# Kernel optimization log

Measured on AMD Instinct MI355X. Metric: run time of the kernel, lower is better.

## Reference

```python
import jax, jax.numpy as jnp
from jax import lax
import numpy as np

HIDDEN = 40
NUM_LAYERS = 7
B, H, W = 16, 64, 64
KS = 7
PAD = KS // 2  # 3

# mask for conv_2d type 'A': zero rows below center, zero right-of-center in
# the center row, and zero the center tap itself
_m = np.ones((1, 1, KS, KS), np.float32)
_m[:, :, PAD + 1:, :] = 0
_m[:, :, PAD, PAD + 1:] = 0
_m[:, :, PAD, PAD] = 0
MASK_A = jnp.asarray(_m)


def conv2d(x, w, pad):
    return lax.conv_general_dilated(x, w, (1, 1), pad,
                                    dimension_numbers=('NCHW', 'OIHW', 'NCHW'))


def setup_inputs() -> dict:
    key = jax.random.key(0)
    ks = jax.random.split(key, 12)
    s = 0.05
    return {
        'input_tensor': jax.random.normal(ks[0], (B, 1, H, W), jnp.float32),
        'target_tensor': jax.random.normal(ks[1], (B, 1, H, W), jnp.float32),
        # masked conv_2d(7,1,80) applied to target
        'w_is': jax.random.normal(ks[2], (2 * HIDDEN, 1, KS, KS), jnp.float32) * s,
        'b_is': jnp.ones((2 * HIDDEN,), jnp.float32),
        # conv_i_s: Conv2d(1, 80, 7, pad 3)
        'w_cis': jax.random.normal(ks[3], (2 * HIDDEN, 1, KS, KS), jnp.float32) * s,
        'b_cis': jax.random.normal(ks[4], (2 * HIDDEN,), jnp.float32) * s,
        # row convs: Conv2d(40, 40, [1,3], pad [0,1])
        'w_rh': jax.random.normal(ks[5], (HIDDEN, HIDDEN, 1, 3), jnp.float32) * s,
        'b_rh': jax.random.normal(ks[6], (HIDDEN,), jnp.float32) * s,
        'w_rc': jax.random.normal(ks[7], (HIDDEN, HIDDEN, 1, 3), jnp.float32) * s,
        'b_rc': jax.random.normal(ks[8], (HIDDEN,), jnp.float32) * s,
        # per-layer cell 1x1 convs: 40 -> 160, stacked over layers
        'w_cell': jax.random.normal(ks[9], (NUM_LAYERS, 4 * HIDDEN, HIDDEN), jnp.float32) * s,
        'b_cell': jax.random.normal(ks[10], (NUM_LAYERS, 4 * HIDDEN), jnp.float32) * s,
        # conv_out: Conv2d(40, 256, 1)
        'w_out': jax.random.normal(ks[11], (256, HIDDEN), jnp.float32) * s,
        'b_out': jnp.zeros((256,), jnp.float32),
    }


def reference(input_tensor, target_tensor, w_is, b_is, w_cis, b_cis,
              w_rh, b_rh, w_rc, b_rc, w_cell, b_cell, w_out, b_out):
    same7 = ((PAD, PAD), (PAD, PAD))
    # i_s = cat([conv_i_s(input), masked_conv(target)], dim=1) -> [B, 160, H, W]
    i_s_input = conv2d(input_tensor, w_cis, same7) + b_cis[None, :, None, None]
    i_s_target = conv2d(target_tensor, w_is * MASK_A, same7) + b_is[None, :, None, None]
    i_s = jnp.concatenate([i_s_input, i_s_target], axis=1)

    h0 = jnp.zeros((B, HIDDEN, 1, W), i_s.dtype)
    c0 = jnp.zeros((B, HIDDEN, 1, W), i_s.dtype)

    def step(carry, x_t):  # x_t: [B, 160, 1, W]
        h, c = carry
        h = conv2d(h, w_rh, ((0, 0), (1, 1))) + b_rh[None, :, None, None]
        c = conv2d(c, w_rc, ((0, 0), (1, 1))) + b_rc[None, :, None, None]
        for l in range(NUM_LAYERS):
            h_conv = jnp.einsum('oc,bcrw->borw', w_cell[l], h) + b_cell[l][None, :, None, None]
            combined = x_t + h_conv
            cc_i, cc_f, cc_o, cc_g = jnp.split(combined, 4, axis=1)
            i = jax.nn.sigmoid(cc_i)
            f = jax.nn.sigmoid(cc_f)
            o = jax.nn.sigmoid(cc_o)
            g = jnp.tanh(cc_g)
            c = f * c + i * g
            h = o * jnp.tanh(c)
        return (h, c), h

    xs = jnp.moveaxis(i_s, 2, 0)[:, :, :, None, :]  # [H, B, 160, 1, W]
    _, hs = lax.scan(step, (h0, c0), xs)            # hs: [H, B, 40, 1, W]
    hidden = jnp.moveaxis(hs[:, :, :, 0, :], 0, 2)  # [B, 40, H, W]
    out = jnp.einsum('oc,bchw->bohw', w_out, hidden) + b_out[None, :, None, None]
    return jax.nn.relu(out)
```

## Files before the change

kernel.cpp:

```cpp
#include <hip/hip_runtime.h>


typedef __bf16 bf16x8 __attribute__((ext_vector_type(8)));
typedef __bf16 bf16x4 __attribute__((ext_vector_type(4)));
typedef float  f32x4  __attribute__((ext_vector_type(4)));

#define SC1 (-1.44269504089f)
#define SC2 (-2.88539008178f)

#define STP 56
#define HLS 896
#define CWS 17

#define BARRIER_LGKM() __asm__ volatile("s_waitcnt lgkmcnt(0)\ns_barrier" ::: "memory")

__global__ __launch_bounds__(256) void prep_kernel(
        const float* __restrict__ wcell, const float* __restrict__ wrh,
        const float* __restrict__ wrc, const float* __restrict__ bcell,
        const float* __restrict__ brh, const float* __restrict__ brc,
        const float* __restrict__ w_out, const float* __restrict__ b_out,
        __bf16* __restrict__ wsA) {
    int i = blockIdx.x * 256 + threadIdx.x;
    if (i >= 137216) return;
    float val = 0.0f;
    if (i < 35840) {
        int j = i & 7, lane = (i >> 3) & 63, lm = i >> 9;
        int mt = lm % 10, l = lm / 10;
        int k = (lane >> 4) * 8 + j, m = lane & 15, r = m & 3;
        int row = r * 40 + 4 * mt + (m >> 2);
        val = wcell[(l * 160 + row) * 40 + k] * (r == 3 ? SC2 : SC1);
    } else if (i < 71680) {
        int i2 = i - 35840;
        int j = i2 & 7, lane = (i2 >> 3) & 63, lm = i2 >> 9;
        int mt = lm % 10, l = lm / 10;
        int k = 32 + (lane >> 4) * 8 + j, m = lane & 15, r = m & 3;
        int row = r * 40 + 4 * mt + (m >> 2);
        float s = (r == 3 ? SC2 : SC1);
        if (k < 40)       val = wcell[(l * 160 + row) * 40 + k] * s;
        else if (k == 40) val = bcell[l * 160 + row] * s;
    } else if (i < 80896) {
        int i3 = i - 71680;
        int j = i3 & 7, lane = (i3 >> 3) & 63, idx = i3 >> 9;
        int mtc = idx % 3, t2 = idx / 3, dx = t2 % 3, cv = t2 / 3;
        int k = (lane >> 4) * 8 + j;
        int ch = 16 * mtc + (lane & 15);
        const float* w = cv ? wrc : wrh;
        if (ch < 40) val = w[(ch * 40 + k) * 3 + dx];
    } else if (i < 90112) {
        int i4 = i - 80896;
        int j = i4 & 7, lane = (i4 >> 3) & 63, idx = i4 >> 9;
        int mtc = idx % 3, t2 = idx / 3, dx = t2 % 3, cv = t2 / 3;
        int k = 32 + (lane >> 4) * 8 + j;
        int ch = 16 * mtc + (lane & 15);
        if (ch < 40) {
            const float* w = cv ? wrc : wrh;
            if (k < 40)                    val = w[(ch * 40 + k) * 3 + dx];
            else if (k == 40 && dx == 1)   val = (cv ? brc : brh)[ch];
        }
    } else if (i < 105472) {
        int i5 = i - 90112;
        int j = i5 & 7, lane = (i5 >> 3) & 63, idx = i5 >> 9;
        int mt = idx % 10, dx = idx / 10;
        int k = (lane >> 4) * 8 + j, m = lane & 15, r = m & 3;
        int row = r * 40 + 4 * mt + (m >> 2);
        float s = (r == 3 ? SC2 : SC1);
        float acc = 0.0f;
        for (int mm = 0; mm < 40; mm++)
            acc = __builtin_fmaf(wcell[row * 40 + mm],
                                 wrh[(mm * 40 + k) * 3 + dx], acc);
        val = acc * s;
    } else if (i < 120832) {
        int i6 = i - 105472;
        int j = i6 & 7, lane = (i6 >> 3) & 63, idx = i6 >> 9;
        int mt = idx % 10, dx = idx / 10;
        int k = 32 + (lane >> 4) * 8 + j, m = lane & 15, r = m & 3;
        int row = r * 40 + 4 * mt + (m >> 2);
        float s = (r == 3 ? SC2 : SC1);
        if (k < 40) {
            float acc = 0.0f;
            for (int mm = 0; mm < 40; mm++)
                acc = __builtin_fmaf(wcell[row * 40 + mm],
                                     wrh[(mm * 40 + k) * 3 + dx], acc);
            val = acc * s;
        } else if (k == 40 && dx == 1) {
            float acc = bcell[row];
            for (int mm = 0; mm < 40; mm++)
                acc = __builtin_fmaf(wcell[row * 40 + mm], brh[mm], acc);
            val = acc * s;
        }
    } else if (i < 129024) {
        int i7 = i - 120832;
        int j = i7 & 7, lane = (i7 >> 3) & 63, ot = i7 >> 9;
        int k = (lane >> 4) * 8 + j;
        int o = ot * 16 + (lane & 15);
        val = w_out[o * 40 + k];
    } else {
        int i8 = i - 129024;
        int j = i8 & 7, lane = (i8 >> 3) & 63, ot = i8 >> 9;
        int k = 32 + (lane >> 4) * 8 + j;
        int o = ot * 16 + (lane & 15);
        if (k < 40)       val = w_out[o * 40 + k];
        else if (k == 40) val = b_out[o];
    }
    wsA[i] = (__bf16)val;
}

__global__ __launch_bounds__(256) void conv7_kernel(
        const float* __restrict__ inp, const float* __restrict__ tgt,
        const float* __restrict__ w_is, const float* __restrict__ b_is,
        const float* __restrict__ w_cis, const float* __restrict__ b_cis,
        float* __restrict__ x_ws) {
    int b = blockIdx.x >> 6, y = blockIdx.x & 63;
    int tid = threadIdx.x, qq = tid >> 6, w = tid & 63;
    const float* ib = inp + b * 4096;
    const float* tb = tgt + b * 4096;
    float pin[7][7], ptg[4][7];
#pragma unroll
    for (int dy = 0; dy < 7; dy++) {
        int yy = y + dy - 3;
#pragma unroll
        for (int dx = 0; dx < 7; dx++) {
            int xx = w + dx - 3;
            bool ok = (yy >= 0 && yy < 64 && xx >= 0 && xx < 64);
            pin[dy][dx] = ok ? ib[yy * 64 + xx] : 0.0f;
            if (dy < 4) ptg[dy][dx] = ok ? tb[yy * 64 + xx] : 0.0f;
        }
    }
    int g = w >> 4, l16 = w & 15;
    for (int j = 0; j < 10; j++) {
        int cc = 4 * j + qq;
        int ccu = __builtin_amdgcn_readfirstlane(cc);
        float a0 = b_cis[ccu], a1 = b_cis[40 + ccu];
        float a2 = b_is[ccu], a3 = b_is[40 + ccu];
        const float* w0 = w_cis + ccu * 49;
        const float* w1 = w_cis + (40 + ccu) * 49;
        const float* w2 = w_is + ccu * 49;
        const float* w3 = w_is + (40 + ccu) * 49;
#pragma unroll
        for (int dy = 0; dy < 7; dy++)
#pragma unroll
            for (int dx = 0; dx < 7; dx++) {
                a0 = __builtin_fmaf(w0[dy * 7 + dx], pin[dy][dx], a0);
                a1 = __builtin_fmaf(w1[dy * 7 + dx], pin[dy][dx], a1);
            }
#pragma unroll
        for (int dy = 0; dy < 3; dy++)
#pragma unroll
            for (int dx = 0; dx < 7; dx++) {
                a2 = __builtin_fmaf(w2[dy * 7 + dx], ptg[dy][dx], a2);
                a3 = __builtin_fmaf(w3[dy * 7 + dx], ptg[dy][dx], a3);
            }
#pragma unroll
        for (int dx = 0; dx < 3; dx++) {
            a2 = __builtin_fmaf(w2[21 + dx], ptg[3][dx], a2);
            a3 = __builtin_fmaf(w3[21 + dx], ptg[3][dx], a3);
        }
        size_t idx = (size_t)((((b * 64 + y) * 4 + g) * 10 + j) * 4 + qq) * 64
                     + l16 * 4;
        *(f32x4*)&x_ws[idx] = f32x4{a0 * SC1, a1 * SC1, a2 * SC1, a3 * SC2};
    }
}

__global__ __launch_bounds__(640, 1) void rnn_kernel(
        const float* __restrict__ x_ws, const __bf16* __restrict__ wsA,
        unsigned long long* __restrict__ halo_ws, float* __restrict__ out) {
    __shared__ __align__(16) __bf16 hC[18 * STP + 64];
    __shared__ __align__(16) __bf16 cC[18 * STP + 64];
    __shared__ __align__(16) __bf16 hL[2 * HLS + 32];
    __shared__ float cwf[40 * CWS];
    __shared__ unsigned cflag[4];

    const int bid = blockIdx.x, g = bid >> 4, b = bid & 15;
    const int tid = threadIdx.x, wv = tid >> 6, lane = tid & 63;
    const int q = lane >> 4, l16 = lane & 15, cc = 4 * wv + q;
    const int W0 = g * 16;

    for (int i = tid; i < 536; i += 640) {
        ((float*)hC)[i] = 0.0f;
        ((float*)cC)[i] = 0.0f;
    }
    for (int i = tid; i < 912; i += 640)
        ((float*)hL)[i] = 0.0f;
    for (int i = tid; i < 40 * CWS; i += 640) cwf[i] = 0.0f;
    if (tid < 4) cflag[tid] = 0xFFFFFFFFu;
    __syncthreads();
    if (tid < 18) { hC[tid * STP + 40] = (__bf16)1.0f; cC[tid * STP + 40] = (__bf16)1.0f; }
    if (tid < 32) hL[(tid >> 4) * HLS + (tid & 15) * STP + 40] = (__bf16)1.0f;
    __syncthreads();

    bf16x8 a0c[6], a1c[6];
#pragma unroll
    for (int l = 1; l < 7; l++) {
        a0c[l - 1] = *(const bf16x8*)&wsA[((l * 10 + wv) * 64 + lane) * 8];
        a1c[l - 1] = *(const bf16x8*)&wsA[35840 + ((l * 10 + wv) * 64 + lane) * 8];
    }
    bf16x8 f0c[3], f1c[3];
#pragma unroll
    for (int dx = 0; dx < 3; dx++) {
        f0c[dx] = *(const bf16x8*)&wsA[90112 + ((dx * 10 + wv) * 64 + lane) * 8];
        f1c[dx] = *(const bf16x8*)&wsA[105472 + ((dx * 10 + wv) * 64 + lane) * 8];
    }
    bf16x8 cva0[3], cva1[3];
    if (wv >= 3 && wv < 6) {
        int mtc = wv - 3;
#pragma unroll
        for (int dx = 0; dx < 3; dx++) {
            int it = (3 + dx) * 3 + mtc;
            cva0[dx] = *(const bf16x8*)&wsA[71680 + (it * 64 + lane) * 8];
            cva1[dx] = *(const bf16x8*)&wsA[80896 + (it * 64 + lane) * 8];
        }
    }
    bf16x8 o0c[2], o1c[2];
    if (wv < 8) {
#pragma unroll
        for (int tt = 0; tt < 2; tt++) {
            int ot = 2 * wv + tt;
            o0c[tt] = *(const bf16x8*)&wsA[120832 + (ot * 64 + lane) * 8];
            o1c[tt] = *(const bf16x8*)&wsA[129024 + (ot * 64 + lane) * 8];
        }
    }

    float c_reg = 0.0f;
    const size_t xstride = 10240;
    const size_t xbase0 = (size_t)(b * 64) * xstride
        + (((size_t)g * 10 + wv) * 4 + q) * 64 + l16 * 4;
    f32x4 xv = *(const f32x4*)&x_ws[xbase0];

    for (int t = 0; t < 64; t++) {
        f32x4 xn = xv;
        if (t < 63) xn = *(const f32x4*)&x_ws[xbase0 + (size_t)(t + 1) * xstride];

        if (wv >= 3 && wv < 6) {
            f32x4 ac = f32x4{0.f, 0.f, 0.f, 0.f};
#pragma unroll
            for (int dx = 0; dx < 3; dx++) {
                bf16x8 b0 = *(const bf16x8*)&cC[(l16 + dx) * STP + q * 8];
                bf16x8 b1 = *(const bf16x8*)&cC[(l16 + dx) * STP + 32 + q * 8];
                ac = __builtin_amdgcn_mfma_f32_16x16x32_bf16(cva0[dx], b0, ac, 0, 0, 0);
                ac = __builtin_amdgcn_mfma_f32_16x16x32_bf16(cva1[dx], b1, ac, 0, 0, 0);
            }
            int mtc = wv - 3, ch0 = 16 * mtc + 4 * q;
            if (ch0 < 40) {
#pragma unroll
                for (int r = 0; r < 4; r++) cwf[(ch0 + r) * CWS + l16] = ac[r];
            }
            __asm__ volatile("s_waitcnt lgkmcnt(0)" ::: "memory");
            if (lane == 0)
                __hip_atomic_store(&cflag[mtc], (unsigned)t,
                                   __ATOMIC_RELAXED, __HIP_MEMORY_SCOPE_WORKGROUP);
        }

        f32x4 acc0 = f32x4{0.f, 0.f, 0.f, 0.f};
#pragma unroll
        for (int dx = 0; dx < 3; dx++) {
            bf16x8 b0 = *(const bf16x8*)&hC[(l16 + dx) * STP + q * 8];
            bf16x8 b1 = *(const bf16x8*)&hC[(l16 + dx) * STP + 32 + q * 8];
            acc0 = __builtin_amdgcn_mfma_f32_16x16x32_bf16(f0c[dx], b0, acc0, 0, 0, 0);
            acc0 = __builtin_amdgcn_mfma_f32_16x16x32_bf16(f1c[dx], b1, acc0, 0, 0, 0);
        }

        if (t > 0 && wv < 8) {
            int y = t - 1;
            bf16x8 bo0 = *(const bf16x8*)&hC[(l16 + 1) * STP + q * 8];
            bf16x8 bo1 = *(const bf16x8*)&hC[(l16 + 1) * STP + 32 + q * 8];
#pragma unroll
            for (int tt = 0; tt < 2; tt++) {
                f32x4 oa = __builtin_amdgcn_mfma_f32_16x16x32_bf16(
                    o0c[tt], bo0, f32x4{0.f, 0.f, 0.f, 0.f}, 0, 0, 0);
                oa = __builtin_amdgcn_mfma_f32_16x16x32_bf16(o1c[tt], bo1, oa, 0, 0, 0);
                int o0 = (2 * wv + tt) * 16 + 4 * q;
#pragma unroll
                for (int r = 0; r < 4; r++)
                    out[((size_t)(b * 256 + o0 + r) * 64 + y) * 64 + W0 + l16] =
                        fmaxf(oa[r], 0.0f);
            }
        }

        {
            int jj = wv >> 2;
            while (__hip_atomic_load(&cflag[jj], __ATOMIC_RELAXED,
                                     __HIP_MEMORY_SCOPE_WORKGROUP) != (unsigned)t)
                __builtin_amdgcn_s_sleep(1);
            __asm__ volatile("" ::: "memory");
        }

#pragma unroll
        for (int l = 0; l < 7; l++) {
            f32x4 acc;
            if (l == 0) {
                acc = acc0;
                c_reg = cwf[cc * CWS + l16];
            } else {
                const __bf16* hb = &hL[(l & 1) * HLS];
                bf16x8 b0 = *(const bf16x8*)&hb[l16 * STP + q * 8];
                bf16x8 b1 = *(const bf16x8*)&hb[l16 * STP + 32 + q * 8];
                acc = __builtin_amdgcn_mfma_f32_16x16x32_bf16(
                    a0c[l - 1], b0, f32x4{0.f, 0.f, 0.f, 0.f}, 0, 0, 0);
                acc = __builtin_amdgcn_mfma_f32_16x16x32_bf16(a1c[l - 1], b1, acc, 0, 0, 0);
            }
            float Ei = __builtin_amdgcn_exp2f(fminf(acc[0] + xv[0], 44.f));
            float Ef = __builtin_amdgcn_exp2f(fminf(acc[1] + xv[1], 44.f));
            float Eo = __builtin_amdgcn_exp2f(fminf(acc[2] + xv[2], 44.f));
            float Eg = __builtin_amdgcn_exp2f(fminf(acc[3] + xv[3], 44.f));
            float f = __builtin_amdgcn_rcpf(1.0f + Ef);
            float ig = (1.0f - Eg) * __builtin_amdgcn_rcpf((1.0f + Ei) * (1.0f + Eg));
            float c = __builtin_fmaf(f, c_reg, ig);
            c_reg = c;
            float Ec = __builtin_amdgcn_exp2f(fminf(SC2 * c, 44.f));
            float h = (1.0f - Ec) * __builtin_amdgcn_rcpf((1.0f + Eo) * (1.0f + Ec));
            if (l < 6) {
                hL[((l + 1) & 1) * HLS + l16 * STP + cc] = (__bf16)h;
                BARRIER_LGKM();
            } else {
                hC[(l16 + 1) * STP + cc] = (__bf16)h;
                cC[(l16 + 1) * STP + cc] = (__bf16)c;
                if (t < 63) {
                    unsigned short h16 = __builtin_bit_cast(unsigned short, (__bf16)h);
                    unsigned short c16 = __builtin_bit_cast(unsigned short, (__bf16)c);
                    unsigned long long v = ((unsigned long long)(unsigned)t << 32)
                        | ((unsigned)c16 << 16) | (unsigned)h16;
                    if (l16 == 0 && g > 0)
                        __hip_atomic_store(
                            &halo_ws[((bid * 2 + 0) * 2 + (t & 1)) * 40 + cc], v,
                            __ATOMIC_RELAXED, __HIP_MEMORY_SCOPE_AGENT);
                    if (l16 == 15 && g < 3)
                        __hip_atomic_store(
                            &halo_ws[((bid * 2 + 1) * 2 + (t & 1)) * 40 + cc], v,
                            __ATOMIC_RELAXED, __HIP_MEMORY_SCOPE_AGENT);
                }
            }
        }

        if (t < 63) {
            if (wv == 8 && g > 0 && lane < 40) {
                const unsigned long long* src =
                    &halo_ws[(((bid - 16) * 2 + 1) * 2 + (t & 1)) * 40 + lane];
                unsigned long long v = __hip_atomic_load(
                    src, __ATOMIC_RELAXED, __HIP_MEMORY_SCOPE_AGENT);
                while ((unsigned)(v >> 32) != (unsigned)t) {
                    __builtin_amdgcn_s_sleep(1);
                    v = __hip_atomic_load(src, __ATOMIC_RELAXED,
                                          __HIP_MEMORY_SCOPE_AGENT);
                }
                hC[lane] = __builtin_bit_cast(__bf16, (unsigned short)(v & 0xffffu));
                cC[lane] = __builtin_bit_cast(__bf16, (unsigned short)((v >> 16) & 0xffffu));
            }
            if (wv == 9 && g < 3 && lane < 40) {
                const unsigned long long* src =
                    &halo_ws[(((bid + 16) * 2 + 0) * 2 + (t & 1)) * 40 + lane];
                unsigned long long v = __hip_atomic_load(
                    src, __ATOMIC_RELAXED, __HIP_MEMORY_SCOPE_AGENT);
                while ((unsigned)(v >> 32) != (unsigned)t) {
                    __builtin_amdgcn_s_sleep(1);
                    v = __hip_atomic_load(src, __ATOMIC_RELAXED,
                                          __HIP_MEMORY_SCOPE_AGENT);
                }
                hC[17 * STP + lane] = __builtin_bit_cast(__bf16, (unsigned short)(v & 0xffffu));
                cC[17 * STP + lane] = __builtin_bit_cast(__bf16, (unsigned short)((v >> 16) & 0xffffu));
            }
        }
        BARRIER_LGKM();
        xv = xn;
    }

    if (wv < 8) {
        bf16x8 bo0 = *(const bf16x8*)&hC[(l16 + 1) * STP + q * 8];
        bf16x8 bo1 = *(const bf16x8*)&hC[(l16 + 1) * STP + 32 + q * 8];
#pragma unroll
        for (int tt = 0; tt < 2; tt++) {
            f32x4 oa = __builtin_amdgcn_mfma_f32_16x16x32_bf16(
                o0c[tt], bo0, f32x4{0.f, 0.f, 0.f, 0.f}, 0, 0, 0);
            oa = __builtin_amdgcn_mfma_f32_16x16x32_bf16(o1c[tt], bo1, oa, 0, 0, 0);
            int o0 = (2 * wv + tt) * 16 + 4 * q;
#pragma unroll
            for (int r = 0; r < 4; r++)
                out[((size_t)(b * 256 + o0 + r) * 64 + 63) * 64 + W0 + l16] =
                    fmaxf(oa[r], 0.0f);
        }
    }
}

extern "C" void kernel_launch(void* const* d_in, const int* in_sizes, int n_in,
                              void* d_out, int out_size, void* d_ws,
                              size_t ws_size, hipStream_t stream) {
    const float* input  = (const float*)d_in[0];
    const float* target = (const float*)d_in[1];
    const float* w_is   = (const float*)d_in[2];
    const float* b_is   = (const float*)d_in[3];
    const float* w_cis  = (const float*)d_in[4];
    const float* b_cis  = (const float*)d_in[5];
    const float* w_rh   = (const float*)d_in[6];
    const float* b_rh   = (const float*)d_in[7];
    const float* w_rc   = (const float*)d_in[8];
    const float* b_rc   = (const float*)d_in[9];
    const float* w_cell = (const float*)d_in[10];
    const float* b_cell = (const float*)d_in[11];
    const float* w_out  = (const float*)d_in[12];
    const float* b_out  = (const float*)d_in[13];
    float* out = (float*)d_out;

    char* ws = (char*)d_ws;
    float*              x_ws    = (float*)ws;
    __bf16*             wsA     = (__bf16*)(ws + 41943040);
    unsigned long long* halo_ws = (unsigned long long*)(ws + 42217472);

    prep_kernel<<<536, 256, 0, stream>>>(w_cell, w_rh, w_rc, b_cell, b_rh,
                                         b_rc, w_out, b_out, wsA);
    conv7_kernel<<<1024, 256, 0, stream>>>(input, target, w_is, b_is, w_cis,
                                           b_cis, x_ws);
    rnn_kernel<<<64, 640, 0, stream>>>(x_ws, wsA, halo_ws, out);
}
```

Baseline: 366.6 us.

## Fuse weight prep and 7x7 conv into one launch with per-channel sliding-row blocks

Merges the weight-packing kernel and the 7x7 input conv kernel into a single launch, with blocks 640 and above doing the weight prep. The conv part is remapped so each block handles one batch and one channel across all rows, with each wave processing 8 consecutive rows. Input rows are kept in a sliding register window, so only one new row is loaded per output row, and the channel weights become block-uniform. This removes one kernel launch and cuts redundant loads, at the cost of more register pressure and a different parallel decomposition.

```diff
diff --git a/kernel.cpp b/kernel.cpp
--- a/kernel.cpp
+++ b/kernel.cpp
@@ -14,128 +14,147 @@
 
 #define BARRIER_LGKM() __asm__ volatile("s_waitcnt lgkmcnt(0)\ns_barrier" ::: "memory")
 
-__global__ __launch_bounds__(256) void prep_kernel(
+__global__ __launch_bounds__(512) void convprep_kernel(
+        const float* __restrict__ inp, const float* __restrict__ tgt,
+        const float* __restrict__ w_is, const float* __restrict__ b_is,
+        const float* __restrict__ w_cis, const float* __restrict__ b_cis,
         const float* __restrict__ wcell, const float* __restrict__ wrh,
         const float* __restrict__ wrc, const float* __restrict__ bcell,
         const float* __restrict__ brh, const float* __restrict__ brc,
         const float* __restrict__ w_out, const float* __restrict__ b_out,
-        __bf16* __restrict__ wsA) {
-    int i = blockIdx.x * 256 + threadIdx.x;
-    if (i >= 137216) return;
-    float val = 0.0f;
-    if (i < 35840) {
-        int j = i & 7, lane = (i >> 3) & 63, lm = i >> 9;
-        int mt = lm % 10, l = lm / 10;
-        int k = (lane >> 4) * 8 + j, m = lane & 15, r = m & 3;
-        int row = r * 40 + 4 * mt + (m >> 2);
-        val = wcell[(l * 160 + row) * 40 + k] * (r == 3 ? SC2 : SC1);
-    } else if (i < 71680) {
-        int i2 = i - 35840;
-        int j = i2 & 7, lane = (i2 >> 3) & 63, lm = i2 >> 9;
-        int mt = lm % 10, l = lm / 10;
-        int k = 32 + (lane >> 4) * 8 + j, m = lane & 15, r = m & 3;
-        int row = r * 40 + 4 * mt + (m >> 2);
-        float s = (r == 3 ? SC2 : SC1);
-        if (k < 40)       val = wcell[(l * 160 + row) * 40 + k] * s;
-        else if (k == 40) val = bcell[l * 160 + row] * s;
-    } else if (i < 80896) {
-        int i3 = i - 71680;
-        int j = i3 & 7, lane = (i3 >> 3) & 63, idx = i3 >> 9;
-        int mtc = idx % 3, t2 = idx / 3, dx = t2 % 3, cv = t2 / 3;
-        int k = (lane >> 4) * 8 + j;
-        int ch = 16 * mtc + (lane & 15);
-        const float* w = cv ? wrc : wrh;
-        if (ch < 40) val = w[(ch * 40 + k) * 3 + dx];
-    } else if (i < 90112) {
-        int i4 = i - 80896;
-        int j = i4 & 7, lane = (i4 >> 3) & 63, idx = i4 >> 9;
-        int mtc = idx % 3, t2 = idx / 3, dx = t2 % 3, cv = t2 / 3;
-        int k = 32 + (lane >> 4) * 8 + j;
-        int ch = 16 * mtc + (lane & 15);
-        if (ch < 40) {
+        float* __restrict__ x_ws, __bf16* __restrict__ wsA) {
+    const int bidx = blockIdx.x;
+    const int tid = threadIdx.x;
+    if (bidx >= 640) {
+        int i = (bidx - 640) * 512 + tid;
+        if (i >= 137216) return;
+        float val = 0.0f;
+        if (i < 35840) {
+            int j = i & 7, lane = (i >> 3) & 63, lm = i >> 9;
+            int mt = lm % 10, l = lm / 10;
+            int k = (lane >> 4) * 8 + j, m = lane & 15, r = m & 3;
+            int row = r * 40 + 4 * mt + (m >> 2);
+            val = wcell[(l * 160 + row) * 40 + k] * (r == 3 ? SC2 : SC1);
+        } else if (i < 71680) {
+            int i2 = i - 35840;
+            int j = i2 & 7, lane = (i2 >> 3) & 63, lm = i2 >> 9;
+            int mt = lm % 10, l = lm / 10;
+            int k = 32 + (lane >> 4) * 8 + j, m = lane & 15, r = m & 3;
+            int row = r * 40 + 4 * mt + (m >> 2);
+            float s = (r == 3 ? SC2 : SC1);
+            if (k < 40)       val = wcell[(l * 160 + row) * 40 + k] * s;
+            else if (k == 40) val = bcell[l * 160 + row] * s;
+        } else if (i < 80896) {
+            int i3 = i - 71680;
+            int j = i3 & 7, lane = (i3 >> 3) & 63, idx = i3 >> 9;
+            int mtc = idx % 3, t2 = idx / 3, dx = t2 % 3, cv = t2 / 3;
+            int k = (lane >> 4) * 8 + j;
+            int ch = 16 * mtc + (lane & 15);
             const float* w = cv ? wrc : wrh;
-            if (k < 40)                    val = w[(ch * 40 + k) * 3 + dx];
-            else if (k == 40 && dx == 1)   val = (cv ? brc : brh)[ch];
-        }
-    } else if (i < 105472) {
-        int i5 = i - 90112;
-        int j = i5 & 7, lane = (i5 >> 3) & 63, idx = i5 >> 9;
-        int mt = idx % 10, dx = idx / 10;
-        int k = (lane >> 4) * 8 + j, m = lane & 15, r = m & 3;
-        int row = r * 40 + 4 * mt + (m >> 2);
-        float s = (r == 3 ? SC2 : SC1);
-        float acc = 0.0f;
-        for (int mm = 0; mm < 40; mm++)
-            acc = __builtin_fmaf(wcell[row * 40 + mm],
-                                 wrh[(mm * 40 + k) * 3 + dx], acc);
-        val = acc * s;
-    } else if (i < 120832) {
-        int i6 = i - 105472;
-        int j = i6 & 7, lane = (i6 >> 3) & 63, idx = i6 >> 9;
-        int mt = idx % 10, dx = idx / 10;
-        int k = 32 + (lane >> 4) * 8 + j, m = lane & 15, r = m & 3;
-        int row = r * 40 + 4 * mt + (m >> 2);
-        float s = (r == 3 ? SC2 : SC1);
-        if (k < 40) {
+            if (ch < 40) val = w[(ch * 40 + k) * 3 + dx];
+        } else if (i < 90112) {
+            int i4 = i - 80896;
+            int j = i4 & 7, lane = (i4 >> 3) & 63, idx = i4 >> 9;
+            int mtc = idx % 3, t2 = idx / 3, dx = t2 % 3, cv = t2 / 3;
+            int k = 32 + (lane >> 4) * 8 + j;
+            int ch = 16 * mtc + (lane & 15);
+            if (ch < 40) {
+                const float* w = cv ? wrc : wrh;
+                if (k < 40)                    val = w[(ch * 40 + k) * 3 + dx];
+                else if (k == 40 && dx == 1)   val = (cv ? brc : brh)[ch];
+            }
+        } else if (i < 105472) {
+            int i5 = i - 90112;
+            int j = i5 & 7, lane = (i5 >> 3) & 63, idx = i5 >> 9;
+            int mt = idx % 10, dx = idx / 10;
+            int k = (lane >> 4) * 8 + j, m = lane & 15, r = m & 3;
+            int row = r * 40 + 4 * mt + (m >> 2);
+            float s = (r == 3 ? SC2 : SC1);
             float acc = 0.0f;
             for (int mm = 0; mm < 40; mm++)
                 acc = __builtin_fmaf(wcell[row * 40 + mm],
                                      wrh[(mm * 40 + k) * 3 + dx], acc);
             val = acc * s;
-        } else if (k == 40 && dx == 1) {
-            float acc = bcell[row];
-            for (int mm = 0; mm < 40; mm++)
-                acc = __builtin_fmaf(wcell[row * 40 + mm], brh[mm], acc);
-            val = acc * s;
-        }
-    } else if (i < 129024) {
-        int i7 = i - 120832;
-        int j = i7 & 7, lane = (i7 >> 3) & 63, ot = i7 >> 9;
-        int k = (lane >> 4) * 8 + j;
-        int o = ot * 16 + (lane & 15);
-        val = w_out[o * 40 + k];
-    } else {
-        int i8 = i - 129024;
-        int j = i8 & 7, lane = (i8 >> 3) & 63, ot = i8 >> 9;
-        int k = 32 + (lane >> 4) * 8 + j;
-        int o = ot * 16 + (lane & 15);
-        if (k < 40)       val = w_out[o * 40 + k];
-        else if (k == 40) val = b_out[o];
-    }
-    wsA[i] = (__bf16)val;
-}
-
-__global__ __launch_bounds__(256) void conv7_kernel(
-        const float* __restrict__ inp, const float* __restrict__ tgt,
-        const float* __restrict__ w_is, const float* __restrict__ b_is,
-        const float* __restrict__ w_cis, const float* __restrict__ b_cis,
-        float* __restrict__ x_ws) {
-    int b = blockIdx.x >> 6, y = blockIdx.x & 63;
-    int tid = threadIdx.x, qq = tid >> 6, w = tid & 63;
+        } else if (i < 120832) {
+            int i6 = i - 105472;
+            int j = i6 & 7, lane = (i6 >> 3) & 63, idx = i6 >> 9;
+            int mt = idx % 10, dx = idx / 10;
+            int k = 32 + (lane >> 4) * 8 + j, m = lane & 15, r = m & 3;
+            int row = r * 40 + 4 * mt + (m >> 2);
+            float s = (r == 3 ? SC2 : SC1);
+            if (k < 40) {
+                float acc = 0.0f;
+                for (int mm = 0; mm < 40; mm++)
+                    acc = __builtin_fmaf(wcell[row * 40 + mm],
+                                         wrh[(mm * 40 + k) * 3 + dx], acc);
+                val = acc * s;
+            } else if (k == 40 && dx == 1) {
+                float acc = bcell[row];
+                for (int mm = 0; mm < 40; mm++)
+                    acc = __builtin_fmaf(wcell[row * 40 + mm], brh[mm], acc);
+                val = acc * s;
+            }
+        } else if (i < 129024) {
+            int i7 = i - 120832;
+            int j = i7 & 7, lane = (i7 >> 3) & 63, ot = i7 >> 9;
+            int k = (lane >> 4) * 8 + j;
+            int o = ot * 16 + (lane & 15);
+            val = w_out[o * 40 + k];
+        } else {
+            int i8 = i - 129024;
+            int j = i8 & 7, lane = (i8 >> 3) & 63, ot = i8 >> 9;
+            int k = 32 + (lane >> 4) * 8 + j;
+            int o = ot * 16 + (lane & 15);
+            if (k < 40)       val = w_out[o * 40 + k];
+            else if (k == 40) val = b_out[o];
+        }
+        wsA[i] = (__bf16)val;
+        return;
+    }
+    const int b = bidx / 40, cc = bidx - b * 40;
+    const int wv = tid >> 6, x = tid & 63;
+    const int y0 = wv * 8;
     const float* ib = inp + b * 4096;
     const float* tb = tgt + b * 4096;
+    const float* w0 = w_cis + cc * 49;
+    const float* w1 = w_cis + (40 + cc) * 49;
+    const float* w2 = w_is + cc * 49;
+    const float* w3 = w_is + (40 + cc) * 49;
+    const float bias0 = b_cis[cc], bias1 = b_cis[40 + cc];
+    const float bias2 = b_is[cc],  bias3 = b_is[40 + cc];
+    const int g = x >> 4, l16 = x & 15;
+    const int jj = cc >> 2, qq = cc & 3;
+
     float pin[7][7], ptg[4][7];
-#pragma unroll
-    for (int dy = 0; dy < 7; dy++) {
-        int yy = y + dy - 3;
+    auto ldrow = [&](const float* base, int yy, float* dst) {
 #pragma unroll
         for (int dx = 0; dx < 7; dx++) {
-            int xx = w + dx - 3;
+            int xx = x + dx - 3;
             bool ok = (yy >= 0 && yy < 64 && xx >= 0 && xx < 64);
-            pin[dy][dx] = ok ? ib[yy * 64 + xx] : 0.0f;
-            if (dy < 4) ptg[dy][dx] = ok ? tb[yy * 64 + xx] : 0.0f;
-        }
-    }
-    int g = w >> 4, l16 = w & 15;
-    for (int j = 0; j < 10; j++) {
-        int cc = 4 * j + qq;
-        int ccu = __builtin_amdgcn_readfirstlane(cc);
-        float a0 = b_cis[ccu], a1 = b_cis[40 + ccu];
-        float a2 = b_is[ccu], a3 = b_is[40 + ccu];
-        const float* w0 = w_cis + ccu * 49;
-        const float* w1 = w_cis + (40 + ccu) * 49;
-        const float* w2 = w_is + ccu * 49;
-        const float* w3 = w_is + (40 + ccu) * 49;
+            dst[dx] = ok ? base[yy * 64 + xx] : 0.0f;
+        }
+    };
+#pragma unroll
+    for (int r = 0; r < 7; r++) ldrow(ib, y0 + r - 3, pin[r]);
+#pragma unroll
+    for (int r = 0; r < 4; r++) ldrow(tb, y0 + r - 3, ptg[r]);
+
+#pragma unroll
+    for (int iy = 0; iy < 8; iy++) {
+        const int y = y0 + iy;
+        if (iy > 0) {
+#pragma unroll
+            for (int r = 0; r < 6; r++)
+#pragma unroll
+                for (int dx = 0; dx < 7; dx++) pin[r][dx] = pin[r + 1][dx];
+            ldrow(ib, y + 3, pin[6]);
+#pragma unroll
+            for (int r = 0; r < 3; r++)
+#pragma unroll
+                for (int dx = 0; dx < 7; dx++) ptg[r][dx] = ptg[r + 1][dx];
+            ldrow(tb, y, ptg[3]);
+        }
+        float a0 = bias0, a1 = bias1, a2 = bias2, a3 = bias3;
 #pragma unroll
         for (int dy = 0; dy < 7; dy++)
 #pragma unroll
@@ -155,7 +174,7 @@
             a2 = __builtin_fmaf(w2[21 + dx], ptg[3][dx], a2);
             a3 = __builtin_fmaf(w3[21 + dx], ptg[3][dx], a3);
         }
-        size_t idx = (size_t)((((b * 64 + y) * 4 + g) * 10 + j) * 4 + qq) * 64
+        size_t idx = (size_t)((((b * 64 + y) * 4 + g) * 10 + jj) * 4 + qq) * 64
                      + l16 * 4;
         *(f32x4*)&x_ws[idx] = f32x4{a0 * SC1, a1 * SC1, a2 * SC1, a3 * SC2};
     }
@@ -404,9 +423,9 @@
     __bf16*             wsA     = (__bf16*)(ws + 41943040);
     unsigned long long* halo_ws = (unsigned long long*)(ws + 42217472);
 
-    prep_kernel<<<536, 256, 0, stream>>>(w_cell, w_rh, w_rc, b_cell, b_rh,
-                                         b_rc, w_out, b_out, wsA);
-    conv7_kernel<<<1024, 256, 0, stream>>>(input, target, w_is, b_is, w_cis,
-                                           b_cis, x_ws);
+    convprep_kernel<<<908, 512, 0, stream>>>(input, target, w_is, b_is,
+                                             w_cis, b_cis, w_cell, w_rh,
+                                             w_rc, b_cell, b_rh, b_rc,
+                                             w_out, b_out, x_ws, wsA);
     rnn_kernel<<<64, 640, 0, stream>>>(x_ws, wsA, halo_ws, out);
 }
```

Result: no change. 370.9 us (+1.2%).
